# Optimization experiments

Measured on AMD Instinct MI355X. Metric: run time of the kernel, lower is better.

Reference implementation:

```python
import jax, jax.numpy as jnp
import numpy as np

DIM = 4096
N_HEAD = 32
N_KV_HEAD = 8
HEAD_DIM = DIM // N_HEAD  # 128
B, T = 2, 2048


def _rope_freqs(T, head_dim, theta=10000.0):
    inv = 1.0 / (theta ** (np.arange(0, head_dim, 2, dtype=np.float32) / head_dim))
    t = np.arange(T, dtype=np.float32)
    ang = np.outer(t, inv)  # [T, head_dim/2]
    return jnp.asarray(np.stack([np.cos(ang), np.sin(ang)], axis=-1))  # [T, hd/2, 2]


def setup_inputs() -> dict:
    key = jax.random.key(0)
    ks = jax.random.split(key, 5)
    s = 1.0 / np.sqrt(DIM)
    return {
        "x": jax.random.normal(ks[0], (B, T, DIM), dtype=jnp.float32),
        "freqs_cis": _rope_freqs(T, HEAD_DIM),
        "wq": jax.random.normal(ks[1], (DIM, N_HEAD * HEAD_DIM), dtype=jnp.float32) * s,
        "wk": jax.random.normal(ks[2], (DIM, N_KV_HEAD * HEAD_DIM), dtype=jnp.float32) * s,
        "wv": jax.random.normal(ks[3], (DIM, N_KV_HEAD * HEAD_DIM), dtype=jnp.float32) * s,
        "wo": jax.random.normal(ks[4], (DIM, DIM), dtype=jnp.float32) * s,
    }


def _apply_rotary(x, freqs_cis):
    # x: [B, T, H, head_dim]; freqs_cis: [T, head_dim/2, 2]
    xs = x.reshape(*x.shape[:-1], -1, 2)  # [B, T, H, hd/2, 2]
    fc = freqs_cis[None, :, None, :, :]   # [1, T, 1, hd/2, 2]
    real = xs[..., 0] * fc[..., 0] - xs[..., 1] * fc[..., 1]
    imag = xs[..., 1] * fc[..., 0] + xs[..., 0] * fc[..., 1]
    return jnp.stack([real, imag], axis=-1).reshape(x.shape)


def reference(x, freqs_cis, wq, wk, wv, wo):
    Bx, Tx, C = x.shape
    q = (x @ wq).reshape(Bx, Tx, N_HEAD, HEAD_DIM)
    k = (x @ wk).reshape(Bx, Tx, N_KV_HEAD, HEAD_DIM)
    v = (x @ wv).reshape(Bx, Tx, N_KV_HEAD, HEAD_DIM)
    q = _apply_rotary(q, freqs_cis)
    k = _apply_rotary(k, freqs_cis)
    # [B, H, T, hd]
    q = q.transpose(0, 2, 1, 3)
    k = k.transpose(0, 2, 1, 3)
    v = v.transpose(0, 2, 1, 3)
    # GQA: expand kv heads to match query heads
    rep = N_HEAD // N_KV_HEAD
    k = jnp.repeat(k, rep, axis=1)
    v = jnp.repeat(v, rep, axis=1)
    scale = 1.0 / np.sqrt(HEAD_DIM)
    scores = jnp.einsum("bhqd,bhkd->bhqk", q, k) * scale
    causal = jnp.tril(jnp.ones((Tx, Tx), dtype=bool))
    scores = jnp.where(causal[None, None], scores, jnp.float32(-1e30))
    attn = jax.nn.softmax(scores, axis=-1)
    y = jnp.einsum("bhqk,bhkd->bhqd", attn, v)
    y = y.transpose(0, 2, 1, 3).reshape(Bx, Tx, C)
    return y @ wo
```

## Files before the change

kernel.cpp:

```cpp
#include <hip/hip_runtime.h>

#define DIM  4096
#define NH   32
#define NKV  8
#define HD   128
#define BSZ  2
#define TSEQ 2048

typedef __bf16 bf16x8 __attribute__((ext_vector_type(8)));
typedef unsigned short ushort8v __attribute__((ext_vector_type(8)));
typedef float f32x4 __attribute__((ext_vector_type(4)));

typedef void GV __attribute__((address_space(1)));
typedef void LV __attribute__((address_space(3)));

__device__ __forceinline__ unsigned short f2bf(float f) {
  unsigned u = __builtin_bit_cast(unsigned, f);
  u += 0x7FFFu + ((u >> 16) & 1u);
  return (unsigned short)(u >> 16);
}
__device__ __forceinline__ float bf2f(unsigned short b) {
  unsigned u = ((unsigned)b) << 16;
  return __builtin_bit_cast(float, u);
}
__device__ __forceinline__ void gload16(const unsigned short* g, unsigned short* l) {
  __builtin_amdgcn_global_load_lds((GV*)g, (LV*)l, 16, 0, 0);
}
__device__ __forceinline__ f32x4 mfma16(bf16x8 a, bf16x8 b, f32x4 c) {
  return __builtin_amdgcn_mfma_f32_16x16x32_bf16(a, b, c, 0, 0, 0);
}
__device__ __forceinline__ bf16x8 lds8(const unsigned short* p) {
  return __builtin_bit_cast(bf16x8, *(const ushort8v*)p);
}

__global__ void detect_dtype(const unsigned int* __restrict__ fc, int* __restrict__ flag) {
  if (threadIdx.x == 0 && blockIdx.x == 0)
    *flag = (fc[0] == 0x3F800000u) ? 0 : 1;
}

__global__ void cast_x(const void* __restrict__ src, unsigned short* __restrict__ dst,
                       const int* __restrict__ flag) {
  long t = (long)blockIdx.x * 256 + threadIdx.x;
  if (*flag) {
    ((uint2*)dst)[t] = ((const uint2*)src)[t];
  } else {
    float4 f = ((const float4*)src)[t];
    ushort4 o;
    o.x = f2bf(f.x); o.y = f2bf(f.y); o.z = f2bf(f.z); o.w = f2bf(f.w);
    ((ushort4*)dst)[t] = o;
  }
}

__global__ __launch_bounds__(256) void transpose64(const void* __restrict__ src,
                                                   unsigned short* __restrict__ dst,
                                                   int R, int C, const int* __restrict__ flag) {
  __shared__ unsigned short tile[64][68];
  const int isbf = *flag;
  const int tid = threadIdx.x;
  const int c0g = blockIdx.x * 64, r0g = blockIdx.y * 64;
  const int cc = (tid & 15) * 4;
  if (isbf) {
    const unsigned short* s = (const unsigned short*)src;
#pragma unroll
    for (int it = 0; it < 4; ++it) {
      const int r = it * 16 + (tid >> 4);
      ushort4 v = *(const ushort4*)(s + (long)(r0g + r) * C + c0g + cc);
      *(ushort4*)&tile[r][cc] = v;
    }
  } else {
    const float* s = (const float*)src;
#pragma unroll
    for (int it = 0; it < 4; ++it) {
      const int r = it * 16 + (tid >> 4);
      float4 f = *(const float4*)(s + (long)(r0g + r) * C + c0g + cc);
      ushort4 v;
      v.x = f2bf(f.x); v.y = f2bf(f.y); v.z = f2bf(f.z); v.w = f2bf(f.w);
      *(ushort4*)&tile[r][cc] = v;
    }
  }
  __syncthreads();
#pragma unroll
  for (int it = 0; it < 2; ++it) {
    const int c = (tid >> 3) + it * 32;
    const int r0 = (tid & 7) * 8;
    ushort8v o;
#pragma unroll
    for (int u = 0; u < 8; ++u) o[u] = tile[r0 + u][c];
    *(ushort8v*)(dst + (long)(c0g + c) * R + r0g + r0) = o;
  }
}

__device__ __forceinline__ void gemm256_loop(const unsigned short* __restrict__ A,
                                             const unsigned short* __restrict__ Bt,
                                             unsigned short* As, unsigned short* Bs,
                                             long tileM, long tileN, f32x4 (&acc)[8][4]) {
  const int tid = (int)threadIdx.x;
  const int lane = tid & 63, wave = tid >> 6;
  const int wr = wave >> 2, wc = wave & 3;
  const int lm = lane & 15, quad = lane >> 4;
  const int srow = wave * 8 + (lane >> 3);
  const int schunk = ((lane & 7) ^ (lane >> 3)) * 8;
  const unsigned short* Ag = A + (tileM + srow) * 4096L + schunk;
  const unsigned short* Bg = Bt + (tileN + srow) * 4096L + schunk;
  unsigned short* Al = As + srow * 64 + (lane & 7) * 8;
  unsigned short* Bl = Bs + srow * 64 + (lane & 7) * 8;

  auto stgA = [&](int slot, int h, int tt) {
    const unsigned short* g = Ag + (long)h * 524288L + (long)tt * 64;
    unsigned short* l = Al + slot * 16384 + h * 8192;
    gload16(g, l);
    gload16(g + 262144L, l + 4096);
  };
  auto stgB = [&](int slot, int h, int tt) {
    const unsigned short* g = Bg + (long)h * 524288L + (long)tt * 64;
    unsigned short* l = Bl + slot * 16384 + h * 8192;
    gload16(g, l);
    gload16(g + 262144L, l + 4096);
  };
  auto rdA = [&](int so, int f16, int kk) {
    return lds8(&As[so + (wr * 128 + f16 * 16 + lm) * 64 + (((kk * 4 + quad) ^ (lm & 7)) * 8)]);
  };
  auto rdB = [&](int so, int f16, int kk) {
    return lds8(&Bs[so + (wc * 64 + f16 * 16 + lm) * 64 + (((kk * 4 + quad) ^ (lm & 7)) * 8)]);
  };

  stgB(0, 0, 0); stgB(0, 1, 0); stgA(0, 0, 0); stgA(0, 1, 0);
  stgB(1, 0, 1); stgB(1, 1, 1); stgA(1, 0, 1);
  asm volatile("s_waitcnt vmcnt(6)" ::: "memory");
  __builtin_amdgcn_s_barrier();

#pragma unroll 2
  for (int t = 0; t < 64; ++t) {
    __builtin_amdgcn_sched_barrier(0);
    const int s = t & 1;
    const int so = s * 16384;
    bf16x8 a[4][2], b0[2][2], b1[2][2];
#pragma unroll
    for (int f = 0; f < 4; ++f) { a[f][0] = rdA(so, f, 0); a[f][1] = rdA(so, f, 1); }
#pragma unroll
    for (int f = 0; f < 2; ++f) { b0[f][0] = rdB(so, f, 0); b0[f][1] = rdB(so, f, 1); }
    if (t < 63) stgA(s ^ 1, 1, t + 1);
    __builtin_amdgcn_s_barrier();
    __builtin_amdgcn_s_setprio(1);
#pragma unroll
    for (int mf = 0; mf < 4; ++mf)
#pragma unroll
      for (int nf = 0; nf < 2; ++nf) {
        acc[mf][nf] = mfma16(a[mf][0], b0[nf][0], acc[mf][nf]);
        acc[mf][nf] = mfma16(a[mf][1], b0[nf][1], acc[mf][nf]);
      }
    __builtin_amdgcn_s_setprio(0);
    __builtin_amdgcn_s_barrier();
#pragma unroll
    for (int f = 0; f < 2; ++f) { b1[f][0] = rdB(so, f + 2, 0); b1[f][1] = rdB(so, f + 2, 1); }
    __builtin_amdgcn_s_barrier();
    __builtin_amdgcn_s_setprio(1);
#pragma unroll
    for (int mf = 0; mf < 4; ++mf)
#pragma unroll
      for (int nf = 0; nf < 2; ++nf) {
        acc[mf][nf + 2] = mfma16(a[mf][0], b1[nf][0], acc[mf][nf + 2]);
        acc[mf][nf + 2] = mfma16(a[mf][1], b1[nf][1], acc[mf][nf + 2]);
      }
    __builtin_amdgcn_s_setprio(0);
    __builtin_amdgcn_s_barrier();
#pragma unroll
    for (int f = 0; f < 4; ++f) { a[f][0] = rdA(so, f + 4, 0); a[f][1] = rdA(so, f + 4, 1); }
    if (t < 62) stgB(s, 0, t + 2);
    __builtin_amdgcn_s_barrier();
    __builtin_amdgcn_s_setprio(1);
#pragma unroll
    for (int mf = 0; mf < 4; ++mf)
#pragma unroll
      for (int nf = 0; nf < 2; ++nf) {
        acc[mf + 4][nf] = mfma16(a[mf][0], b0[nf][0], acc[mf + 4][nf]);
        acc[mf + 4][nf] = mfma16(a[mf][1], b0[nf][1], acc[mf + 4][nf]);
      }
    __builtin_amdgcn_s_setprio(0);
    __builtin_amdgcn_s_barrier();
    if (t < 62) { stgB(s, 1, t + 2); stgA(s, 0, t + 2); }
    __builtin_amdgcn_s_barrier();
    __builtin_amdgcn_s_setprio(1);
#pragma unroll
    for (int mf = 0; mf < 4; ++mf)
#pragma unroll
      for (int nf = 0; nf < 2; ++nf) {
        acc[mf + 4][nf + 2] = mfma16(a[mf][0], b1[nf][0], acc[mf + 4][nf + 2]);
        acc[mf + 4][nf + 2] = mfma16(a[mf][1], b1[nf][1], acc[mf + 4][nf + 2]);
      }
    __builtin_amdgcn_s_setprio(0);
    if (t < 62)       asm volatile("s_waitcnt vmcnt(6)" ::: "memory");
    else if (t == 62) asm volatile("s_waitcnt vmcnt(0)" ::: "memory");
    __builtin_amdgcn_s_barrier();
  }
}

__global__ __launch_bounds__(512, 2) void gemm_qkv8(const unsigned short* __restrict__ A,
                                                    const unsigned short* __restrict__ Bt,
                                                    const void* __restrict__ fcv,
                                                    const int* __restrict__ flag,
                                                    unsigned short* __restrict__ qo,
                                                    unsigned short* __restrict__ ko,
                                                    unsigned short* __restrict__ vo) {
  __shared__ __align__(16) unsigned short As[2 * 16384];
  __shared__ __align__(16) unsigned short Bs[2 * 16384];
  const int bid = (int)blockIdx.x;
  const int nb2 = (bid & 7) * 48 + (bid >> 3);
  const long tileM = (long)(nb2 / 24) * 256;
  const long tileN = (long)(nb2 % 24) * 256;
  f32x4 acc[8][4] = {};
  gemm256_loop(A, Bt, As, Bs, tileM, tileN, acc);
  const int tid = (int)threadIdx.x;
  const int lane = tid & 63, wave = tid >> 6;
  const int wr = wave >> 2, wc = wave & 3;
  const int lm = lane & 15, quad = lane >> 4;
  const int isbf = *flag;
  const int nb = (int)tileN + wc * 64;
  if (nb < 5120) {
    const int isk = (nb >= 4096);
    unsigned short* dst = isk ? ko : qo;
    const int hpb = isk ? NKV : NH;
    const int coff = isk ? 4096 : 0;
#pragma unroll
    for (int mf = 0; mf < 8; ++mf)
#pragma unroll
      for (int r = 0; r < 4; ++r) {
        const int m = (int)tileM + wr * 128 + mf * 16 + quad * 4 + r;
        const int b = m >> 11, tq = m & (TSEQ - 1);
#pragma unroll
        for (int nf = 0; nf < 4; ++nf) {
          const int n = nb + nf * 16 + lm;
          float val = acc[mf][nf][r];
          float par = __shfl_xor(val, 1);
          const int ip = (n & 127) >> 1;
          const long fo = (long)tq * 64 + ip;
          float cz, sz;
          if (isbf) {
            const unsigned short* fu = (const unsigned short*)fcv;
            cz = bf2f(fu[fo * 2]); sz = bf2f(fu[fo * 2 + 1]);
          } else {
            float2 cs = ((const float2*)fcv)[fo];
            cz = cs.x; sz = cs.y;
          }
          float out = (n & 1) ? (val * cz + par * sz) : (val * cz - par * sz);
          const int h = (n - coff) >> 7, d = n & 127;
          dst[((long)(b * hpb + h) * TSEQ + tq) * HD + d] = f2bf(out);
        }
      }
  } else {
#pragma unroll
    for (int mf = 0; mf < 8; ++mf)
#pragma unroll
      for (int r = 0; r < 4; ++r) {
        const int m = (int)tileM + wr * 128 + mf * 16 + quad * 4 + r;
        const int b = m >> 11, tq = m & (TSEQ - 1);
#pragma unroll
        for (int nf = 0; nf < 4; ++nf) {
          const int n = nb + nf * 16 + lm;
          const int h = (n - 5120) >> 7, d = n & 127;
          vo[((long)(b * NKV + h) * HD + d) * TSEQ + tq] = f2bf(acc[mf][nf][r]);
        }
      }
  }
}

__global__ __launch_bounds__(512, 2) void gemm_wo8(const unsigned short* __restrict__ A,
                                                   const unsigned short* __restrict__ Bt,
                                                   void* __restrict__ Cv,
                                                   const int* __restrict__ flag) {
  __shared__ __align__(16) unsigned short As[2 * 16384];
  __shared__ __align__(16) unsigned short Bs[2 * 16384];
  const int bid = (int)blockIdx.x;
  const int nb2 = (bid & 7) * 32 + (bid >> 3);
  const long tileM = (long)(nb2 >> 4) * 256;
  const long tileN = (long)(nb2 & 15) * 256;
  f32x4 acc[8][4] = {};
  gemm256_loop(A, Bt, As, Bs, tileM, tileN, acc);
  const int tid = (int)threadIdx.x;
  const int lane = tid & 63, wave = tid >> 6;
  const int wr = wave >> 2, wc = wave & 3;
  const int lm = lane & 15, quad = lane >> 4;
  const int obf = *flag;
  const long N = 4096;
  if (obf) {
    unsigned short* C = (unsigned short*)Cv;
#pragma unroll
    for (int mf = 0; mf < 8; ++mf)
#pragma unroll
      for (int nf = 0; nf < 4; ++nf)
#pragma unroll
        for (int r = 0; r < 4; ++r)
          C[(tileM + wr * 128 + mf * 16 + quad * 4 + r) * N + tileN + wc * 64 + nf * 16 + lm] =
              f2bf(acc[mf][nf][r]);
  } else {
    float* C = (float*)Cv;
#pragma unroll
    for (int mf = 0; mf < 8; ++mf)
#pragma unroll
      for (int nf = 0; nf < 4; ++nf)
#pragma unroll
        for (int r = 0; r < 4; ++r)
          C[(tileM + wr * 128 + mf * 16 + quad * 4 + r) * N + tileN + wc * 64 + nf * 16 + lm] =
              acc[mf][nf][r];
  }
}

__global__ __launch_bounds__(256, 3) void flash_attn(const unsigned short* __restrict__ q,
                                                     const unsigned short* __restrict__ k,
                                                     const unsigned short* __restrict__ vT,
                                                     unsigned short* __restrict__ y) {
  __shared__ unsigned short Ks[2][32 * 128];
  __shared__ unsigned short Vs[2][128 * 32];
  __shared__ unsigned short Pl[4][32 * 40];
  const int tid = threadIdx.x;
  const int lane = tid & 63, wave = tid >> 6;
  const int lm = lane & 15, quad = lane >> 4;
  const int bh = blockIdx.y, b = bh >> 5, h = bh & 31, kvh = h >> 2;
  const int qi = (int)gridDim.x - 1 - (int)blockIdx.x;
  const int q0 = qi * 128;
  const unsigned short* Qb = q + ((long)(b * NH + h) * TSEQ + q0 + wave * 32) * HD;
  const unsigned short* Kb = k + (long)(b * NKV + kvh) * TSEQ * HD;
  const unsigned short* Vb = vT + (long)(b * NKV + kvh) * HD * TSEQ;
  bf16x8 qf[2][4];
#pragma unroll
  for (int mi = 0; mi < 2; ++mi)
#pragma unroll
    for (int ks = 0; ks < 4; ++ks)
      qf[mi][ks] = __builtin_bit_cast(bf16x8,
          *(const ushort8v*)(Qb + (mi * 16 + lm) * HD + ks * 32 + quad * 8));
  f32x4 o[2][8] = {};
  float li[2][4] = {};
  const float scale = 0.08838834764831845f;
  const int krow = tid >> 4, kcl = ((tid & 15) ^ (krow & 7)) * 8;
  const int vrow = tid >> 2, vcl = ((tid & 3) ^ ((vrow >> 1) & 3)) * 8;
  const int ktiles = qi * 4 + 4;
  {
    gload16(Kb + krow * HD + kcl, &Ks[0][tid * 8]);
    gload16(Kb + (16 + krow) * HD + kcl, &Ks[0][2048 + tid * 8]);
    gload16(Vb + (long)vrow * TSEQ + vcl, &Vs[0][tid * 8]);
    gload16(Vb + (long)(64 + vrow) * TSEQ + vcl, &Vs[0][2048 + tid * 8]);
  }
  for (int kt = 0; kt < ktiles; ++kt) {
    __syncthreads();
    if (kt + 1 < ktiles) {
      const int bi = (kt + 1) & 1;
      const unsigned short* Kg = Kb + (long)(kt + 1) * 32 * HD;
      gload16(Kg + krow * HD + kcl, &Ks[bi][tid * 8]);
      gload16(Kg + (16 + krow) * HD + kcl, &Ks[bi][2048 + tid * 8]);
      const unsigned short* Vg = Vb + (kt + 1) * 32;
      gload16(Vg + (long)vrow * TSEQ + vcl, &Vs[bi][tid * 8]);
      gload16(Vg + (long)(64 + vrow) * TSEQ + vcl, &Vs[bi][2048 + tid * 8]);
    }
    const unsigned short* KsB = Ks[kt & 1];
    const unsigned short* VsB = Vs[kt & 1];
    f32x4 s[2][2] = {};
#pragma unroll
    for (int ni = 0; ni < 2; ++ni)
#pragma unroll
      for (int ks = 0; ks < 4; ++ks) {
        bf16x8 kf = lds8(&KsB[(ni * 16 + lm) * 128 + ((ks * 4 + quad) ^ (lm & 7)) * 8]);
        s[0][ni] = mfma16(qf[0][ks], kf, s[0][ni]);
        s[1][ni] = mfma16(qf[1][ks], kf, s[1][ni]);
      }
    unsigned short* PlW = &Pl[wave][0];
#pragma unroll
    for (int mi = 0; mi < 2; ++mi)
#pragma unroll
      for (int r = 0; r < 4; ++r) {
        const int qg = q0 + wave * 32 + mi * 16 + quad * 4 + r;
#pragma unroll
        for (int ni = 0; ni < 2; ++ni) {
          const int kg = kt * 32 + ni * 16 + lm;
          float p = (kg <= qg) ? __expf(s[mi][ni][r] * scale) : 0.f;
          li[mi][r] += p;
          PlW[(mi * 16 + quad * 4 + r) * 40 + ni * 16 + lm] = f2bf(p);
        }
      }
    bf16x8 pf0 = lds8(&PlW[lm * 40 + quad * 8]);
    bf16x8 pf1 = lds8(&PlW[(16 + lm) * 40 + quad * 8]);
#pragma unroll
    for (int db = 0; db < 8; ++db) {
      bf16x8 vf = lds8(&VsB[(db * 16 + lm) * 32 + (quad ^ ((lm >> 1) & 3)) * 8]);
      o[0][db] = mfma16(pf0, vf, o[0][db]);
      o[1][db] = mfma16(pf1, vf, o[1][db]);
    }
  }
  float inv[2][4];
#pragma unroll
  for (int mi = 0; mi < 2; ++mi)
#pragma unroll
    for (int r = 0; r < 4; ++r) {
      float l = li[mi][r];
      l += __shfl_xor(l, 1, 16);
      l += __shfl_xor(l, 2, 16);
      l += __shfl_xor(l, 4, 16);
      l += __shfl_xor(l, 8, 16);
      inv[mi][r] = 1.0f / l;
    }
  unsigned short* yo = y + ((long)b * TSEQ + q0 + wave * 32) * DIM + h * 128 + lm;
#pragma unroll
  for (int mi = 0; mi < 2; ++mi)
#pragma unroll
    for (int r = 0; r < 4; ++r) {
      unsigned short* yr = yo + (long)(mi * 16 + quad * 4 + r) * DIM;
#pragma unroll
      for (int db = 0; db < 8; ++db)
        yr[db * 16] = f2bf(o[mi][db][r] * inv[mi][r]);
    }
}

extern "C" void kernel_launch(void* const* d_in, const int* in_sizes, int n_in,
                              void* d_out, int out_size, void* d_ws, size_t ws_size,
                              hipStream_t stream) {
  const void* x  = d_in[0];
  const void* fc = d_in[1];
  const void* wq = d_in[2];
  const void* wk = d_in[3];
  const void* wv = d_in[4];
  const void* wo = d_in[5];
  char* ws = (char*)d_ws;
  int* flag             = (int*)ws;
  unsigned short* xb    = (unsigned short*)(ws + 256);
  unsigned short* wqkvT = xb + 16777216L;
  unsigned short* woT   = wqkvT + 25165824L;
  unsigned short* qb    = woT + 16777216L;
  unsigned short* kb    = qb + 16777216L;
  unsigned short* vb    = kb + 4194304L;
  unsigned short* yb    = xb;

  detect_dtype<<<dim3(1), dim3(64), 0, stream>>>((const unsigned int*)fc, flag);
  cast_x<<<dim3(16384), dim3(256), 0, stream>>>(x, xb, flag);
  transpose64<<<dim3(64, 64), dim3(256), 0, stream>>>(wq, wqkvT, 4096, 4096, flag);
  transpose64<<<dim3(16, 64), dim3(256), 0, stream>>>(wk, wqkvT + 4096L * 4096, 4096, 1024, flag);
  transpose64<<<dim3(16, 64), dim3(256), 0, stream>>>(wv, wqkvT + 5120L * 4096, 4096, 1024, flag);
  transpose64<<<dim3(64, 64), dim3(256), 0, stream>>>(wo, woT, 4096, 4096, flag);
  gemm_qkv8<<<dim3(384), dim3(512), 0, stream>>>(xb, wqkvT, fc, flag, qb, kb, vb);
  flash_attn<<<dim3(16, 64), dim3(256), 0, stream>>>(qb, kb, vb, yb);
  gemm_wo8<<<dim3(256), dim3(512), 0, stream>>>(yb, woT, d_out, flag);
}
```

Baseline: 846.0 us.

## Software-pipeline GEMM main loop with next-tile LDS prefetch into registers

```diff
diff --git a/kernel.cpp b/kernel.cpp
--- a/kernel.cpp
+++ b/kernel.cpp
@@ -125,73 +125,120 @@
   };
 
   stgB(0, 0, 0); stgB(0, 1, 0); stgA(0, 0, 0); stgA(0, 1, 0);
-  stgB(1, 0, 1); stgB(1, 1, 1); stgA(1, 0, 1);
-  asm volatile("s_waitcnt vmcnt(6)" ::: "memory");
+  stgB(1, 0, 1); stgB(1, 1, 1); stgA(1, 0, 1); stgA(1, 1, 1);
+  asm volatile("s_waitcnt vmcnt(8)" ::: "memory");
+  __builtin_amdgcn_sched_barrier(0);
   __builtin_amdgcn_s_barrier();
 
+  bf16x8 a0[4][2], a1[4][2], b01[2][2], b23[2][2];
+#pragma unroll
+  for (int f = 0; f < 4; ++f) { a0[f][0] = rdA(0, f, 0); a0[f][1] = rdA(0, f, 1); }
+#pragma unroll
+  for (int f = 0; f < 2; ++f) { b01[f][0] = rdB(0, f, 0); b01[f][1] = rdB(0, f, 1); }
+
 #pragma unroll 2
-  for (int t = 0; t < 64; ++t) {
-    __builtin_amdgcn_sched_barrier(0);
-    const int s = t & 1;
-    const int so = s * 16384;
-    bf16x8 a[4][2], b0[2][2], b1[2][2];
-#pragma unroll
-    for (int f = 0; f < 4; ++f) { a[f][0] = rdA(so, f, 0); a[f][1] = rdA(so, f, 1); }
-#pragma unroll
-    for (int f = 0; f < 2; ++f) { b0[f][0] = rdB(so, f, 0); b0[f][1] = rdB(so, f, 1); }
-    if (t < 63) stgA(s ^ 1, 1, t + 1);
-    __builtin_amdgcn_s_barrier();
+  for (int t = 0; t < 63; ++t) {
+    const int so = (t & 1) * 16384, sn = so ^ 16384, sl = t & 1;
+    b23[0][0] = rdB(so, 2, 0); b23[0][1] = rdB(so, 2, 1);
+    b23[1][0] = rdB(so, 3, 0); b23[1][1] = rdB(so, 3, 1);
+    asm volatile("s_waitcnt lgkmcnt(4)" ::: "memory");
+    __builtin_amdgcn_sched_barrier(0);
     __builtin_amdgcn_s_setprio(1);
 #pragma unroll
     for (int mf = 0; mf < 4; ++mf)
 #pragma unroll
       for (int nf = 0; nf < 2; ++nf) {
-        acc[mf][nf] = mfma16(a[mf][0], b0[nf][0], acc[mf][nf]);
-        acc[mf][nf] = mfma16(a[mf][1], b0[nf][1], acc[mf][nf]);
+        acc[mf][nf] = mfma16(a0[mf][0], b01[nf][0], acc[mf][nf]);
+        acc[mf][nf] = mfma16(a0[mf][1], b01[nf][1], acc[mf][nf]);
       }
     __builtin_amdgcn_s_setprio(0);
     __builtin_amdgcn_s_barrier();
 #pragma unroll
-    for (int f = 0; f < 2; ++f) { b1[f][0] = rdB(so, f + 2, 0); b1[f][1] = rdB(so, f + 2, 1); }
+    for (int f = 0; f < 4; ++f) { a1[f][0] = rdA(so, f + 4, 0); a1[f][1] = rdA(so, f + 4, 1); }
+    asm volatile("s_waitcnt lgkmcnt(8)" ::: "memory");
+    __builtin_amdgcn_sched_barrier(0);
+    __builtin_amdgcn_s_setprio(1);
+#pragma unroll
+    for (int mf = 0; mf < 4; ++mf)
+#pragma unroll
+      for (int nf = 0; nf < 2; ++nf) {
+        acc[mf][nf + 2] = mfma16(a0[mf][0], b23[nf][0], acc[mf][nf + 2]);
+        acc[mf][nf + 2] = mfma16(a0[mf][1], b23[nf][1], acc[mf][nf + 2]);
+      }
+    __builtin_amdgcn_s_setprio(0);
+    asm volatile("s_waitcnt vmcnt(0)" ::: "memory");
+    __builtin_amdgcn_sched_barrier(0);
     __builtin_amdgcn_s_barrier();
+    bf16x8 na[4][2], nb[2][2];
+#pragma unroll
+    for (int f = 0; f < 4; ++f) { na[f][0] = rdA(sn, f, 0); na[f][1] = rdA(sn, f, 1); }
+#pragma unroll
+    for (int f = 0; f < 2; ++f) { nb[f][0] = rdB(sn, f, 0); nb[f][1] = rdB(sn, f, 1); }
+    if (t < 62) { stgB(sl, 0, t + 2); stgB(sl, 1, t + 2); }
+    asm volatile("s_waitcnt lgkmcnt(12)" ::: "memory");
+    __builtin_amdgcn_sched_barrier(0);
     __builtin_amdgcn_s_setprio(1);
 #pragma unroll
     for (int mf = 0; mf < 4; ++mf)
 #pragma unroll
       for (int nf = 0; nf < 2; ++nf) {
-        acc[mf][nf + 2] = mfma16(a[mf][0], b1[nf][0], acc[mf][nf + 2]);
-        acc[mf][nf + 2] = mfma16(a[mf][1], b1[nf][1], acc[mf][nf + 2]);
+        acc[mf + 4][nf] = mfma16(a1[mf][0], b01[nf][0], acc[mf + 4][nf]);
+        acc[mf + 4][nf] = mfma16(a1[mf][1], b01[nf][1], acc[mf + 4][nf]);
       }
     __builtin_amdgcn_s_setprio(0);
     __builtin_amdgcn_s_barrier();
-#pragma unroll
-    for (int f = 0; f < 4; ++f) { a[f][0] = rdA(so, f + 4, 0); a[f][1] = rdA(so, f + 4, 1); }
-    if (t < 62) stgB(s, 0, t + 2);
-    __builtin_amdgcn_s_barrier();
+    if (t < 62) { stgA(sl, 0, t + 2); stgA(sl, 1, t + 2); }
     __builtin_amdgcn_s_setprio(1);
 #pragma unroll
     for (int mf = 0; mf < 4; ++mf)
 #pragma unroll
       for (int nf = 0; nf < 2; ++nf) {
-        acc[mf + 4][nf] = mfma16(a[mf][0], b0[nf][0], acc[mf + 4][nf]);
-        acc[mf + 4][nf] = mfma16(a[mf][1], b0[nf][1], acc[mf + 4][nf]);
+        acc[mf + 4][nf + 2] = mfma16(a1[mf][0], b23[nf][0], acc[mf + 4][nf + 2]);
+        acc[mf + 4][nf + 2] = mfma16(a1[mf][1], b23[nf][1], acc[mf + 4][nf + 2]);
       }
     __builtin_amdgcn_s_setprio(0);
     __builtin_amdgcn_s_barrier();
-    if (t < 62) { stgB(s, 1, t + 2); stgA(s, 0, t + 2); }
-    __builtin_amdgcn_s_barrier();
-    __builtin_amdgcn_s_setprio(1);
-#pragma unroll
-    for (int mf = 0; mf < 4; ++mf)
-#pragma unroll
-      for (int nf = 0; nf < 2; ++nf) {
-        acc[mf + 4][nf + 2] = mfma16(a[mf][0], b1[nf][0], acc[mf + 4][nf + 2]);
-        acc[mf + 4][nf + 2] = mfma16(a[mf][1], b1[nf][1], acc[mf + 4][nf + 2]);
-      }
-    __builtin_amdgcn_s_setprio(0);
-    if (t < 62)       asm volatile("s_waitcnt vmcnt(6)" ::: "memory");
-    else if (t == 62) asm volatile("s_waitcnt vmcnt(0)" ::: "memory");
-    __builtin_amdgcn_s_barrier();
+#pragma unroll
+    for (int f = 0; f < 4; ++f) { a0[f][0] = na[f][0]; a0[f][1] = na[f][1]; }
+#pragma unroll
+    for (int f = 0; f < 2; ++f) { b01[f][0] = nb[f][0]; b01[f][1] = nb[f][1]; }
+  }
+
+  {
+    const int so = 16384;
+    b23[0][0] = rdB(so, 2, 0); b23[0][1] = rdB(so, 2, 1);
+    b23[1][0] = rdB(so, 3, 0); b23[1][1] = rdB(so, 3, 1);
+    asm volatile("s_waitcnt lgkmcnt(4)" ::: "memory");
+    __builtin_amdgcn_sched_barrier(0);
+#pragma unroll
+    for (int mf = 0; mf < 4; ++mf)
+#pragma unroll
+      for (int nf = 0; nf < 2; ++nf) {
+        acc[mf][nf] = mfma16(a0[mf][0], b01[nf][0], acc[mf][nf]);
+        acc[mf][nf] = mfma16(a0[mf][1], b01[nf][1], acc[mf][nf]);
+      }
+#pragma unroll
+    for (int f = 0; f < 4; ++f) { a1[f][0] = rdA(so, f + 4, 0); a1[f][1] = rdA(so, f + 4, 1); }
+    asm volatile("s_waitcnt lgkmcnt(8)" ::: "memory");
+    __builtin_amdgcn_sched_barrier(0);
+#pragma unroll
+    for (int mf = 0; mf < 4; ++mf)
+#pragma unroll
+      for (int nf = 0; nf < 2; ++nf) {
+        acc[mf][nf + 2] = mfma16(a0[mf][0], b23[nf][0], acc[mf][nf + 2]);
+        acc[mf][nf + 2] = mfma16(a0[mf][1], b23[nf][1], acc[mf][nf + 2]);
+      }
+    asm volatile("s_waitcnt lgkmcnt(0)" ::: "memory");
+    __builtin_amdgcn_sched_barrier(0);
+#pragma unroll
+    for (int mf = 0; mf < 4; ++mf)
+#pragma unroll
+      for (int nf = 0; nf < 2; ++nf) {
+        acc[mf + 4][nf] = mfma16(a1[mf][0], b01[nf][0], acc[mf + 4][nf]);
+        acc[mf + 4][nf] = mfma16(a1[mf][1], b01[nf][1], acc[mf + 4][nf]);
+        acc[mf + 4][nf + 2] = mfma16(a1[mf][0], b23[nf][0], acc[mf + 4][nf + 2]);
+        acc[mf + 4][nf + 2] = mfma16(a1[mf][1], b23[nf][1], acc[mf + 4][nf + 2]);
+      }
   }
 }
 
```

After: 966.6 us. 1.14x slower.
